# Optimization experiments

Hardware: AMD Instinct MI355X
Metric: run time of the kernel (lower is better)

The kernel has to match this reference:

```python
import jax, jax.numpy as jnp
import numpy as np

B, P, N, H, W = 8, 4096, 1024, 1024, 1024


def setup_inputs() -> dict:
    key = jax.random.key(0)
    k1, k2, k3, k4 = jax.random.split(key, 4)
    return {
        "pred_points": jax.random.uniform(k1, (B, P, 2), dtype=jnp.float32),
        "dicts_coords": jax.random.uniform(k2, (B, N, 2), dtype=jnp.float32),
        "dicts_keys": jax.random.randint(k3, (B, N), 0, 1024, dtype=jnp.int64) if jax.config.jax_enable_x64 else jax.random.randint(k3, (B, N), 0, 1024).astype(jnp.int32),
        "masks": jax.random.randint(k4, (B, H, W), 0, 1025).astype(jnp.int32),
    }


def _match_single(U, V, keys, lm):
    # U: [P,2] normalized points, V: [N,2] gt coords, keys: [N] ids, lm: [H,W] label map
    h, w = lm.shape
    x = jnp.clip(jnp.round(U[:, 0] * h).astype(jnp.int32), 0, h - 1)
    y = jnp.clip(jnp.round(U[:, 1] * w).astype(jnp.int32), 0, w - 1)
    labels = lm[x, y]                                   # [P] label at each point
    # inside[j, p] == (mask for gt j covers point p); mask j is label channel keys[j]+1
    inside = labels[None, :] == (keys + 1)[:, None]     # [N,P] bool
    # full euclidean distance matrix gt->points
    D = jnp.sqrt(jnp.sum((V[:, None, :] - U[None, :, :]) ** 2, axis=-1))  # [N,P]
    inside_any = inside.any(axis=0)                     # points inside ANY mask
    avail0 = inside_any
    bg0 = ~inside_any                                   # background points
    idx = jnp.arange(U.shape[0])
    BIG = jnp.asarray(1e30, D.dtype)

    def step(carry, xs):
        avail, bg = carry
        ins_j, d_j = xs
        cand = ins_j & avail
        cnt = cand.sum()
        d_in = jnp.where(cand, d_j, BIG)
        u_in = jnp.argmin(d_in)                         # first-index tiebreak, like list order
        d_bg = jnp.where(bg, d_j, BIG)
        u_bg = jnp.argmin(d_bg)
        has_bg = bg.any()
        use_in = cnt > 0
        u = jnp.where(use_in, u_in, jnp.where(has_bg, u_bg, -1))
        cost = jnp.where(use_in, d_in[u_in], jnp.where(has_bg, d_bg[u_bg], jnp.asarray(0.0, D.dtype)))
        # inside-match consumes u from available; multi-point case dumps others into bg
        avail = jnp.where(use_in, avail & (idx != u_in), avail)
        others = cand & (idx != u_in)
        bg = jnp.where(use_in,
                       jnp.where(cnt > 1, bg | others, bg),
                       jnp.where(has_bg, bg & (idx != u_bg), bg))
        return (avail, bg), (u, cost)

    _, (src, costs) = jax.lax.scan(step, (avail0, bg0), (inside, D))
    tgt = jnp.where(src >= 0, jnp.arange(V.shape[0]), -1)
    return src, tgt, costs.sum()


def reference(pred_points, dicts_coords, dicts_keys, masks):
    # Returns padded matches per batch: src[b,j] = matched point index for gt j (-1 if skipped),
    # tgt[b,j] = j when matched else -1, total_cost[b] = sum of matched distances.
    src, tgt, total_cost = jax.vmap(_match_single)(pred_points, dicts_coords, dicts_keys, masks)
    return src, tgt, total_cost
```

## Files before the change

kernel.cpp:

```cpp
#include <hip/hip_runtime.h>
#include <stdint.h>

#define PPTS 4096
#define NGT  1024
#define HH   1024
#define WW   1024
#define EVPOOL_CAP 3072
#define BGCAP 160
#define RB 12

#define PART_BYTES (8 * 8 * 1025 * 2)
#define LAB_OFF    PART_BYTES
#define SPILL_OFF  (LAB_OFF + 8 * PPTS * 2)
#define SPILL_CAP  2048
#define WS_NEED    (SPILL_OFF + 8 * SPILL_CAP * 2)

typedef unsigned long long u64;

__device__ __forceinline__ float pdist2(float vx, float vy, float ux, float uy) {
    float dx = __fsub_rn(vx, ux);
    float dy = __fsub_rn(vy, uy);
    return __fadd_rn(__fmul_rn(dx, dx), __fmul_rn(dy, dy));
}

__global__ __launch_bounds__(512) void label_kernel(
    const float* __restrict__ pred, const int* __restrict__ masks,
    unsigned short* __restrict__ part, unsigned short* __restrict__ labs)
{
    __shared__ int lh[1025];
    const int blk = blockIdx.x, b = blk >> 3, sb = blk & 7;
    const int t = threadIdx.x;
    lh[t] = 0; lh[t + 512] = 0;
    if (t == 0) lh[1024] = 0;
    __syncthreads();
    const int p = (sb << 9) + t;
    float2 u = ((const float2*)(pred + (size_t)b * PPTS * 2))[p];
    int xi = (int)rintf(__fmul_rn(u.x, 1024.0f));
    int yi = (int)rintf(__fmul_rn(u.y, 1024.0f));
    xi = min(max(xi, 0), HH - 1);
    yi = min(max(yi, 0), WW - 1);
    int lab = (masks + (size_t)b * HH * WW)[xi * WW + yi];
    labs[(size_t)b * PPTS + p] = (unsigned short)lab;
    atomicAdd(&lh[lab], 1);
    __syncthreads();
    unsigned short* Pp = part + (size_t)b * 8200;
    Pp[t * 8 + sb] = (unsigned short)lh[t];
    Pp[(t + 512) * 8 + sb] = (unsigned short)lh[t + 512];
    if (t == 0) Pp[1024 * 8 + sb] = (unsigned short)lh[1024];
}

__global__ __launch_bounds__(1024) void matcher_kernel(
    const float* __restrict__ pred,
    const float* __restrict__ coords,
    const int*   __restrict__ keys,
    const int*   __restrict__ masks,
    float* __restrict__ out,
    const unsigned short* __restrict__ part, const unsigned short* __restrict__ labs,
    unsigned short* __restrict__ spill, int useWs, int B)
{
    __shared__ __align__(16) char regU[32768];
    __shared__ __align__(8)  char regE[8192];
    __shared__ __align__(8)  char regB[8200];
    __shared__ __align__(8)  char regP[2 * EVPOOL_CAP];
    __shared__ __align__(4)  char regS[384];
    __shared__ __align__(8)  char regT[2048];
    __shared__ u64            wScr64[16];
    __shared__ u64            sTot;
    __shared__ unsigned short evAx[1024];
    __shared__ unsigned short occList[NGT];
    __shared__ short          matchU[NGT];
    __shared__ unsigned       bgbits[PPTS / 32];
    __shared__ int            scal[4];
    __shared__ float2         vLds[NGT];
    __shared__ unsigned       cellCnt[1024];
    __shared__ unsigned short cellOf[PPTS];
    __shared__ unsigned short gIdx[PPTS];
    __shared__ unsigned short gP[PPTS];
    __shared__ __align__(16) float2 gC[PPTS];

    float2*         bucketC  = (float2*)regU;
    unsigned short* ldsEnt   = (unsigned short*)regE;
    int*            bEnd     = (int*)regB;
    int*            occA     = ((int*)regB) + 1025;
    u64*            specWin  = (u64*)regB;
    int*            firstOcc = (int*)regP;
    unsigned short* evPool   = (unsigned short*)regP;
    unsigned*       present  = (unsigned*)regS;
    unsigned short* bgListSh = (unsigned short*)regS;
    unsigned short* bSt      = (unsigned short*)regT;
    float2*         vSteps   = (float2*)regT;
    int*   wScrI = (int*)wScr64;
    float* wScrF = (float*)wScr64;

    const int b = blockIdx.x;
    const int t = threadIdx.x;
    const int lane = t & 63, wv = t >> 6;
    const float* Ub = pred   + (size_t)b * PPTS * 2;
    const float2* Ub2 = (const float2*)Ub;
    const float* Vb = coords + (size_t)b * NGT * 2;
    const float2* Vb2 = (const float2*)Vb;
    const int*   Kb = keys   + (size_t)b * NGT;
    unsigned short* evSpillB = spill + (size_t)b * SPILL_CAP;
    const int spillCap = useWs ? SPILL_CAP : 0;

    if (t < PPTS / 32) bgbits[t] = 0;
    if (t == 0) scal[0] = 0;
    cellCnt[t] = 0;
    const int k1 = Kb[t] + 1;
    const float2 vMe = Vb2[t];
    vLds[t] = vMe;
    int lab[4]; float2 up[4];
    #pragma unroll
    for (int i = 0; i < 4; i++) up[i] = Ub2[t + (i << 10)];
    occA[t] = 0; firstOcc[t] = 0x7FFFFFFF;
    if (t == 0) { occA[1024] = 0; firstOcc[1024] = 0x7FFFFFFF; }
    if (t < 33) present[t] = 0;
    if (useWs) {
        const unsigned short* Pb = part + (size_t)b * 8200;
        const uint4 pv = reinterpret_cast<const uint4*>(Pb)[t];
        int s = (int)(pv.x & 0xFFFFu) + (int)(pv.x >> 16)
              + (int)(pv.y & 0xFFFFu) + (int)(pv.y >> 16)
              + (int)(pv.z & 0xFFFFu) + (int)(pv.z >> 16)
              + (int)(pv.w & 0xFFFFu) + (int)(pv.w >> 16);
        bEnd[t] = s;
        if (t == 0) {
            const uint4 p1 = reinterpret_cast<const uint4*>(Pb)[1024];
            bEnd[1024] = (int)(p1.x & 0xFFFFu) + (int)(p1.x >> 16)
                       + (int)(p1.y & 0xFFFFu) + (int)(p1.y >> 16)
                       + (int)(p1.z & 0xFFFFu) + (int)(p1.z >> 16)
                       + (int)(p1.w & 0xFFFFu) + (int)(p1.w >> 16);
        }
        const unsigned short* Lb = labs + (size_t)b * PPTS;
        #pragma unroll
        for (int i = 0; i < 4; i++) lab[i] = Lb[t + (i << 10)];
    } else {
        bEnd[t] = 0;
        if (t == 0) bEnd[1024] = 0;
    }
    __syncthreads();
    atomicOr(&present[k1 >> 5], 1u << (k1 & 31));
    atomicAdd(&occA[k1], 1);
    atomicMin(&firstOcc[k1], t);
    if (!useWs) {
        const int* Mb = masks + (size_t)b * HH * WW;
        #pragma unroll
        for (int i = 0; i < 4; i++) {
            float2 u = up[i];
            int xi = (int)rintf(__fmul_rn(u.x, 1024.0f));
            int yi = (int)rintf(__fmul_rn(u.y, 1024.0f));
            xi = min(max(xi, 0), HH - 1);
            yi = min(max(yi, 0), WW - 1);
            lab[i] = Mb[xi * WW + yi];
            atomicAdd(&bEnd[lab[i]], 1);
        }
    }
    __syncthreads();

    {
        int c0 = bEnd[t], o0 = occA[t];
        bool pr0 = (present[t >> 5] >> (t & 31)) & 1u;
        int bCnt = bEnd[k1];
        int fo   = firstOcc[k1];
        int evc  = (fo == t && bCnt > 0) ? (bCnt - 1) : 0;
        u64 myv = (pr0 ? ((u64)(unsigned)c0 << 32) : ((u64)(unsigned)c0 << 48))
                  | ((u64)(unsigned)evc << 16) | (u64)(unsigned)o0;
        u64 add1 = 0; bool pr1 = false;
        if (t == 1023) {
            int c1 = bEnd[1024], o1 = occA[1024];
            pr1 = present[32] & 1u;
            add1 = (pr1 ? ((u64)(unsigned)c1 << 32) : ((u64)(unsigned)c1 << 48))
                   | (u64)(unsigned)o1;
        }
        u64 tot = myv + add1;
        u64 inc = tot;
        #pragma unroll
        for (int off = 1; off < 64; off <<= 1) {
            u64 n = __shfl_up(inc, off, 64);
            if (lane >= off) inc += n;
        }
        if (lane == 63) wScr64[wv] = inc;
        __syncthreads();
        if (t < 16) {
            u64 v = wScr64[t], inc2 = v;
            #pragma unroll
            for (int off = 1; off < 16; off <<= 1) {
                u64 n = __shfl_up(inc2, off, 64);
                if (t >= off) inc2 += n;
            }
            wScr64[t] = inc2 - v;
            if (t == 15) sTot = inc2;
        }
        __syncthreads();
        u64 excl = wScr64[wv] + inc - tot;
        int nBg0v = (int)(sTot >> 48);
        int bgS = (int)(excl >> 48);
        int prS = (int)((excl >> 32) & 0xFFFF);
        int evS = (int)((excl >> 16) & 0xFFFF);
        int ocS = (int)(excl & 0xFFFF);
        int start0 = pr0 ? (nBg0v + prS) : bgS;
        bEnd[t] = start0;
        occA[t] = ocS;
        evAx[t] = (unsigned short)evS;
        if (t >= 1) bSt[t - 1] = (unsigned short)start0;
        if (t == 1023) {
            u64 ex1 = excl + myv;
            int bgS1 = (int)(ex1 >> 48);
            int prS1 = (int)((ex1 >> 32) & 0xFFFF);
            int start1 = pr1 ? (nBg0v + prS1) : bgS1;
            bEnd[1024] = start1; occA[1024] = (int)(ex1 & 0xFFFF);
            bSt[1023] = (unsigned short)start1;
        }
    }
    __syncthreads();
    const int nBg0  = (int)(sTot >> 48);
    const int totEv = (int)((sTot >> 16) & 0xFFFF);
    const int EVcap = min(EVPOOL_CAP, PPTS - nBg0);

    #pragma unroll
    for (int i = 0; i < 4; i++) {
        int p = t + (i << 10);
        int slot = atomicAdd(&bEnd[lab[i]], 1);
        ldsEnt[slot] = (unsigned short)p;
        bucketC[slot] = up[i];
        if (!((present[lab[i] >> 5] >> (lab[i] & 31)) & 1u)) {
            int cx = min(31, max(0, (int)__fmul_rn(up[i].x, 32.0f)));
            int cy = min(31, max(0, (int)__fmul_rn(up[i].y, 32.0f)));
            int cell = (cx << 5) | cy;
            cellOf[slot] = (unsigned short)cell;
            atomicAdd(&cellCnt[cell], 1u);
        }
    }
    {
        int slot = atomicAdd(&occA[k1], 1);
        occList[slot] = (unsigned short)t;
    }
    __syncthreads();

    float costPartial = 0.0f;
    {
        const int l = t + 1;
        const int os = occA[t], oe = occA[l];
        for (int i = os + 1; i < oe; i++) {
            unsigned short v = occList[i];
            int k = i - 1;
            while (k >= os && occList[k] > v) { occList[k + 1] = occList[k]; k--; }
            occList[k + 1] = v;
        }
        const int bs = bSt[t], be = bEnd[l];
        const int bn = be - bs;
        if (oe > os && bn > 0 && bn <= RB) {
            float rcx[RB], rcy[RB]; int rp[RB];
            #pragma unroll
            for (int k = 0; k < RB; k++)
                if (k < bn) { float2 c = bucketC[bs + k]; rcx[k] = c.x; rcy[k] = c.y;
                              rp[k] = ldsEnt[bs + k]; }
            unsigned cons = 0;
            for (int o = os; o < oe; o++) {
                int j = occList[o];
                float2 v = vLds[j];
                u64 best = ~0ull;
                #pragma unroll
                for (int k = 0; k < RB; k++) {
                    if (k < bn && !((cons >> k) & 1u)) {
                        float d2 = pdist2(v.x, v.y, rcx[k], rcy[k]);
                        u64 pk = ((u64)__float_as_uint(d2) << 24)
                                 | ((u64)(unsigned)rp[k] << 12) | (u64)(unsigned)k;
                        if (pk < best) best = pk;
                    }
                }
                if (best != ~0ull) {
                    int eW = (int)(best & 0xFFFull);
                    matchU[j] = (short)((best >> 12) & 0xFFFull);
                    costPartial = __fadd_rn(costPartial,
                        __fsqrt_rn(__uint_as_float((unsigned)(best >> 24))));
                    cons |= 1u << eW;
                    if (o == os) {
                        int base = evAx[j];
                        #pragma unroll
                        for (int k = 0; k < RB; k++) {
                            if (k < bn && k != eW) {
                                int idx = base + k - (k > eW ? 1 : 0);
                                if (idx < EVcap) evPool[idx] = (unsigned short)(bs + k);
                                else if (idx - EVcap < spillCap)
                                    evSpillB[idx - EVcap] = (unsigned short)rp[k];
                            }
                        }
                    }
                } else matchU[j] = -2;
            }
        } else if (oe > os) {
            u64 cons = 0;
            for (int o = os; o < oe; o++) {
                int j = occList[o];
                float2 v = vLds[j];
                u64 best = ~0ull;
                int avail = 0;
                for (int e = bs; e < be; e++) {
                    int eIdx = e - bs;
                    int p = ldsEnt[e];
                    bool consd;
                    if (eIdx < 64) consd = (cons >> eIdx) & 1ull;
                    else {
                        consd = false;
                        for (int o2 = os; o2 < o; o2++)
                            if ((int)matchU[occList[o2]] == p) { consd = true; break; }
                    }
                    if (consd) continue;
                    avail++;
                    float2 u = bucketC[e];
                    float d2 = pdist2(v.x, v.y, u.x, u.y);
                    u64 pk = ((u64)__float_as_uint(d2) << 24) | ((u64)(unsigned)p << 12)
                             | (u64)(unsigned)eIdx;
                    if (pk < best) best = pk;
                }
                if (avail > 0) {
                    int eW = (int)(best & 0xFFFull);
                    matchU[j] = (short)((best >> 12) & 0xFFFull);
                    costPartial = __fadd_rn(costPartial,
                        __fsqrt_rn(__uint_as_float((unsigned)(best >> 24))));
                    if (eW < 64) cons |= 1ull << eW;
                    if (o == os) {
                        int base = evAx[j], w3 = 0;
                        for (int e = bs; e < be; e++) {
                            if (e - bs == eW) continue;
                            int idx = base + w3;
                            if (idx < EVcap) evPool[idx] = (unsigned short)e;
                            else if (idx - EVcap < spillCap)
                                evSpillB[idx - EVcap] = ldsEnt[e];
                            w3++;
                        }
                    }
                } else matchU[j] = -2;
            }
        }
    }
    __syncthreads();

    {
        bool need = (matchU[t] == (short)-2);
        u64 m = __ballot(need);
        if (lane == 0) wScrI[wv] = __popcll(m);
    }
    __syncthreads();
    if (t < 64) {
        int orig = (t < 16) ? wScrI[t] : 0;
        int v = orig;
        #pragma unroll
        for (int off = 1; off <= 8; off <<= 1) {
            int n = __shfl_up(v, off, 64);
            if (t >= off) v += n;
        }
        if (t < 16) wScrI[t] = v - orig;
        if (t == 15) scal[0] = v;
    }
    __syncthreads();
    {
        bool need = (matchU[t] == (short)-2);
        u64 m = __ballot(need);
        if (need) {
            int rank = __popcll(m & ((1ull << lane) - 1ull));
            int idx = wScrI[wv] + rank;
            if (idx < BGCAP) { bgListSh[idx] = (unsigned short)t; vSteps[idx] = vMe; }
        }
    }
    __syncthreads();

    const int bgCnt = min(scal[0], BGCAP);
    {
        const int nStage = min(totEv, EVcap);
        float2 sc[4]; unsigned short sp[4];
        #pragma unroll
        for (int k = 0; k < 4; k++) {
            int i = t + (k << 10);
            if (i < nStage) { int slot = evPool[i]; sp[k] = ldsEnt[slot]; sc[k] = bucketC[slot]; }
        }
        __syncthreads();
        #pragma unroll
        for (int k = 0; k < 4; k++) {
            int i = t + (k << 10);
            if (i < nStage) {
                ldsEnt[nBg0 + i] = sp[k]; bucketC[nBg0 + i] = sc[k];
                int cx = min(31, max(0, (int)__fmul_rn(sc[k].x, 32.0f)));
                int cy = min(31, max(0, (int)__fmul_rn(sc[k].y, 32.0f)));
                int cell = (cx << 5) | cy;
                cellOf[nBg0 + i] = (unsigned short)cell;
                atomicAdd(&cellCnt[cell], 1u);
            }
        }
    }
    __syncthreads();

    if (bgCnt > 0) {
        const int nT = nBg0 + min(totEv, EVcap);
        {
            unsigned c0 = cellCnt[t];
            unsigned inc = c0;
            #pragma unroll
            for (int off = 1; off < 64; off <<= 1) {
                unsigned n = __shfl_up(inc, off, 64);
                if (lane >= off) inc += n;
            }
            if (lane == 63) wScrI[wv] = (int)inc;
            __syncthreads();
            if (t < 16) {
                int v = wScrI[t], inc2 = v;
                #pragma unroll
                for (int off = 1; off < 16; off <<= 1) {
                    int n = __shfl_up(inc2, off, 64);
                    if (t >= off) inc2 += n;
                }
                wScrI[t] = inc2 - v;
            }
            __syncthreads();
            unsigned excl = (unsigned)wScrI[wv] + inc - c0;
            cellCnt[t] = excl;
            __syncthreads();
        }
        #pragma unroll
        for (int k = 0; k < 4; k++) {
            int i = t + (k << 10);
            if (i < nT) {
                int cell = cellOf[i];
                int slot = (int)atomicAdd(&cellCnt[cell], 1u);
                gIdx[slot] = (unsigned short)i;
                gP[slot]   = ldsEnt[i];
                gC[slot]   = bucketC[i];
            }
        }
        __syncthreads();
        for (int s = wv; s < bgCnt; s += 16) {
            const int js = bgListSh[s];
            const float2 v = vSteps[s];
            const int lim = nBg0 + min((int)evAx[js], EVcap);
            const int cx = min(31, max(0, (int)__fmul_rn(v.x, 32.0f)));
            const int cy = min(31, max(0, (int)__fmul_rn(v.y, 32.0f)));
            u64 best = ~0ull;
            if (lane < 25) {
                int x = cx + (lane / 5) - 2, y = cy + (lane % 5) - 2;
                if ((unsigned)x < 32u && (unsigned)y < 32u) {
                    int c = (x << 5) | y;
                    int beg = c ? (int)cellCnt[c - 1] : 0;
                    int end = (int)cellCnt[c];
                    for (int i2 = beg; i2 < end; i2++) {
                        if (gIdx[i2] < lim) {
                            float2 cc = gC[i2];
                            float d2 = pdist2(v.x, v.y, cc.x, cc.y);
                            u64 pk = ((u64)__float_as_uint(d2) << 32) | gP[i2];
                            if (pk < best) best = pk;
                        }
                    }
                }
            }
            #pragma unroll
            for (int off = 32; off >= 1; off >>= 1) {
                u64 o = __shfl_xor(best, off, 64);
                if (o < best) best = o;
            }
            for (int r = 3; r <= 31; r++) {
                float gap = __fmul_rn((float)(r - 1), 0.03125f) - 1e-6f;
                float bd2 = __uint_as_float((unsigned)(best >> 32));
                if (bd2 < __fmul_rn(gap, gap)) break;
                const int ncells = 8 * r;
                for (int ci = lane; ci < ncells; ci += 64) {
                    int dx, dy;
                    if (ci < 2 * r)           { dx = -r + ci;            dy = -r; }
                    else if (ci < 4 * r)      { dx = r;                  dy = -r + (ci - 2 * r); }
                    else if (ci < 6 * r)      { dx = r - (ci - 4 * r);   dy = r; }
                    else                      { dx = -r;                 dy = r - (ci - 6 * r); }
                    int x = cx + dx, y = cy + dy;
                    if ((unsigned)x < 32u && (unsigned)y < 32u) {
                        int c = (x << 5) | y;
                        int beg = c ? (int)cellCnt[c - 1] : 0;
                        int end = (int)cellCnt[c];
                        for (int i2 = beg; i2 < end; i2++) {
                            if (gIdx[i2] < lim) {
                                float2 cc = gC[i2];
                                float d2 = pdist2(v.x, v.y, cc.x, cc.y);
                                u64 pk = ((u64)__float_as_uint(d2) << 32) | gP[i2];
                                if (pk < best) best = pk;
                            }
                        }
                    }
                }
                #pragma unroll
                for (int off = 32; off >= 1; off >>= 1) {
                    u64 o = __shfl_xor(best, off, 64);
                    if (o < best) best = o;
                }
            }
            const int ne = evAx[js];
            if (ne > EVcap && spillCap > 0) {
                for (int ei = EVcap + lane; ei < ne; ei += 64) {
                    if (ei - EVcap >= spillCap) break;
                    unsigned p = evSpillB[ei - EVcap];
                    float2 c = Ub2[p];
                    float d2 = pdist2(v.x, v.y, c.x, c.y);
                    u64 pk = ((u64)__float_as_uint(d2) << 32) | p;
                    if (pk < best) best = pk;
                }
                #pragma unroll
                for (int off = 32; off >= 1; off >>= 1) {
                    u64 o = __shfl_xor(best, off, 64);
                    if (o < best) best = o;
                }
            }
            if (lane == 0) specWin[s] = best;
        }
    }
    __syncthreads();

    {
        int done = 0;
        for (;;) {
            if (t == 0) scal[3] = bgCnt;
            __syncthreads();
            if (t >= done && t < bgCnt) {
                u64 w = specWin[t];
                if (w != ~0ull) {
                    unsigned p = (unsigned)(w & 0xFFFFFFFFull);
                    bool inval = (bgbits[p >> 5] >> (p & 31)) & 1u;
                    if (!inval) {
                        for (int s2 = done; s2 < t; s2++) {
                            u64 w2 = specWin[s2];
                            if (w2 != ~0ull &&
                                (unsigned)(w2 & 0xFFFFFFFFull) == p) { inval = true; break; }
                        }
                    }
                    if (inval) atomicMin(&scal[3], t);
                }
            }
            __syncthreads();
            const int fs = scal[3];
            if (fs >= bgCnt) break;
            if (t >= done && t < fs) {
                u64 w = specWin[t];
                if (w != ~0ull) {
                    unsigned p = (unsigned)(w & 0xFFFFFFFFull);
                    atomicOr(&bgbits[p >> 5], 1u << (p & 31));
                }
            }
            __syncthreads();
            {
                const int js = bgListSh[fs];
                const float2 v = vSteps[fs];
                const int ne = evAx[js];
                const int lim = nBg0 + min(ne, EVcap);
                u64 best = ~0ull;
                for (int i = t; i < lim; i += 1024) {
                    unsigned p = ldsEnt[i];
                    if (!((bgbits[p >> 5] >> (p & 31)) & 1u)) {
                        float2 c = bucketC[i];
                        float d2 = pdist2(v.x, v.y, c.x, c.y);
                        u64 pk = ((u64)__float_as_uint(d2) << 32) | p;
                        if (pk < best) best = pk;
                    }
                }
                for (int ei = EVcap + t; ei < ne; ei += 1024) {
                    if (ei - EVcap >= spillCap) break;
                    unsigned p = evSpillB[ei - EVcap];
                    if (!((bgbits[p >> 5] >> (p & 31)) & 1u)) {
                        float2 c = Ub2[p];
                        float d2 = pdist2(v.x, v.y, c.x, c.y);
                        u64 pk = ((u64)__float_as_uint(d2) << 32) | p;
                        if (pk < best) best = pk;
                    }
                }
                #pragma unroll
                for (int off = 32; off >= 1; off >>= 1) {
                    u64 o = __shfl_xor(best, off, 64);
                    if (o < best) best = o;
                }
                if (lane == 0) wScr64[wv] = best;
                __syncthreads();
                if (t == 0) {
                    u64 bb = wScr64[0];
                    for (int i = 1; i < 16; i++) if (wScr64[i] < bb) bb = wScr64[i];
                    specWin[fs] = bb;
                    if (bb != ~0ull) {
                        unsigned p = (unsigned)(bb & 0xFFFFFFFFull);
                        bgbits[p >> 5] |= 1u << (p & 31);
                    }
                }
            }
            done = fs + 1;
        }
    }
    if (t < bgCnt) {
        const int js = bgListSh[t];
        u64 w0 = specWin[t];
        if (w0 == ~0ull) matchU[js] = -1;
        else {
            matchU[js] = (short)(w0 & 0xFFFFFFFFull);
            costPartial = __fadd_rn(costPartial,
                __fsqrt_rn(__uint_as_float((unsigned)(w0 >> 32))));
        }
    }
    __syncthreads();

    {
        float cp = costPartial;
        #pragma unroll
        for (int off = 32; off >= 1; off >>= 1) cp += __shfl_xor(cp, off, 64);
        if (lane == 0) wScrF[wv] = cp;
    }
    __syncthreads();
    if (t == 0) {
        float tot = 0.0f;
        for (int i = 0; i < 16; ++i) tot = __fadd_rn(tot, wScrF[i]);
        out[(size_t)2 * B * NGT + b] = tot;
    }
    {
        int u = matchU[t];
        out[(size_t)b * NGT + t] = (float)u;
        out[(size_t)B * NGT + (size_t)b * NGT + t] = (u >= 0) ? (float)t : -1.0f;
    }
}

extern "C" void kernel_launch(void* const* d_in, const int* in_sizes, int n_in,
                              void* d_out, int out_size, void* d_ws, size_t ws_size,
                              hipStream_t stream) {
    const float* pred   = (const float*)d_in[0];
    const float* coords = (const float*)d_in[1];
    const int*   keys   = (const int*)d_in[2];
    const int*   masks  = (const int*)d_in[3];
    float* out = (float*)d_out;
    int B = in_sizes[2] / NGT;
    int useWs = (B == 8 && ws_size >= (size_t)WS_NEED) ? 1 : 0;
    unsigned short* partP  = (unsigned short*)d_ws;
    unsigned short* labsP  = (unsigned short*)((char*)d_ws + LAB_OFF);
    unsigned short* spillP = (unsigned short*)((char*)d_ws + SPILL_OFF);
    if (useWs) {
        label_kernel<<<B * 8, 512, 0, stream>>>(pred, masks, partP, labsP);
    }
    matcher_kernel<<<B, 1024, 0, stream>>>(pred, coords, keys, masks, out,
                                           partP, labsP, spillP, useWs, B);
}
```

Before: 110.3 us.

## Fold label gather and histogram into matcher kernel, drop separate label pass

Removes the separate label_kernel launch and its workspace round-trip. The matcher now gathers mask labels itself, issuing the gathers early so they overlap the shared-memory initialisation, and builds the label histogram with shared atomics. It also reuses the per-lane ballot rank instead of recomputing the ballot. The cost is that the random mask gathers now run on only 8 blocks instead of 64, which may expose more latency.

After: 112.7 us. 2.2% more time.

```diff
diff --git a/kernel.cpp b/kernel.cpp
--- a/kernel.cpp
+++ b/kernel.cpp
@@ -9,11 +9,8 @@
 #define BGCAP 160
 #define RB 12
 
-#define PART_BYTES (8 * 8 * 1025 * 2)
-#define LAB_OFF    PART_BYTES
-#define SPILL_OFF  (LAB_OFF + 8 * PPTS * 2)
 #define SPILL_CAP  2048
-#define WS_NEED    (SPILL_OFF + 8 * SPILL_CAP * 2)
+#define WS_NEED    (8 * SPILL_CAP * 2)
 
 typedef unsigned long long u64;
 
@@ -21,32 +18,6 @@
     float dx = __fsub_rn(vx, ux);
     float dy = __fsub_rn(vy, uy);
     return __fadd_rn(__fmul_rn(dx, dx), __fmul_rn(dy, dy));
-}
-
-__global__ __launch_bounds__(512) void label_kernel(
-    const float* __restrict__ pred, const int* __restrict__ masks,
-    unsigned short* __restrict__ part, unsigned short* __restrict__ labs)
-{
-    __shared__ int lh[1025];
-    const int blk = blockIdx.x, b = blk >> 3, sb = blk & 7;
-    const int t = threadIdx.x;
-    lh[t] = 0; lh[t + 512] = 0;
-    if (t == 0) lh[1024] = 0;
-    __syncthreads();
-    const int p = (sb << 9) + t;
-    float2 u = ((const float2*)(pred + (size_t)b * PPTS * 2))[p];
-    int xi = (int)rintf(__fmul_rn(u.x, 1024.0f));
-    int yi = (int)rintf(__fmul_rn(u.y, 1024.0f));
-    xi = min(max(xi, 0), HH - 1);
-    yi = min(max(yi, 0), WW - 1);
-    int lab = (masks + (size_t)b * HH * WW)[xi * WW + yi];
-    labs[(size_t)b * PPTS + p] = (unsigned short)lab;
-    atomicAdd(&lh[lab], 1);
-    __syncthreads();
-    unsigned short* Pp = part + (size_t)b * 8200;
-    Pp[t * 8 + sb] = (unsigned short)lh[t];
-    Pp[(t + 512) * 8 + sb] = (unsigned short)lh[t + 512];
-    if (t == 0) Pp[1024 * 8 + sb] = (unsigned short)lh[1024];
 }
 
 __global__ __launch_bounds__(1024) void matcher_kernel(
@@ -55,8 +26,7 @@
     const int*   __restrict__ keys,
     const int*   __restrict__ masks,
     float* __restrict__ out,
-    const unsigned short* __restrict__ part, const unsigned short* __restrict__ labs,
-    unsigned short* __restrict__ spill, int useWs, int B)
+    unsigned short* __restrict__ spill, int spillCap, int B)
 {
     __shared__ __align__(16) char regU[32768];
     __shared__ __align__(8)  char regE[8192];
@@ -101,59 +71,37 @@
     const float2* Vb2 = (const float2*)Vb;
     const int*   Kb = keys   + (size_t)b * NGT;
     unsigned short* evSpillB = spill + (size_t)b * SPILL_CAP;
-    const int spillCap = useWs ? SPILL_CAP : 0;
-
+
+    int lab[4]; float2 up[4];
+    #pragma unroll
+    for (int i = 0; i < 4; i++) up[i] = Ub2[t + (i << 10)];
+    const int k1v = Kb[t];
+    const float2 vMe = Vb2[t];
+    const int* Mb = masks + (size_t)b * HH * WW;
+    #pragma unroll
+    for (int i = 0; i < 4; i++) {
+        int xi = (int)rintf(__fmul_rn(up[i].x, 1024.0f));
+        int yi = (int)rintf(__fmul_rn(up[i].y, 1024.0f));
+        xi = min(max(xi, 0), HH - 1);
+        yi = min(max(yi, 0), WW - 1);
+        lab[i] = Mb[xi * WW + yi];
+    }
+    const int k1 = k1v + 1;
     if (t < PPTS / 32) bgbits[t] = 0;
     if (t == 0) scal[0] = 0;
     cellCnt[t] = 0;
-    const int k1 = Kb[t] + 1;
-    const float2 vMe = Vb2[t];
     vLds[t] = vMe;
-    int lab[4]; float2 up[4];
-    #pragma unroll
-    for (int i = 0; i < 4; i++) up[i] = Ub2[t + (i << 10)];
     occA[t] = 0; firstOcc[t] = 0x7FFFFFFF;
-    if (t == 0) { occA[1024] = 0; firstOcc[1024] = 0x7FFFFFFF; }
+    bEnd[t] = 0;
+    if (t == 0) { occA[1024] = 0; firstOcc[1024] = 0x7FFFFFFF; bEnd[1024] = 0; }
     if (t < 33) present[t] = 0;
-    if (useWs) {
-        const unsigned short* Pb = part + (size_t)b * 8200;
-        const uint4 pv = reinterpret_cast<const uint4*>(Pb)[t];
-        int s = (int)(pv.x & 0xFFFFu) + (int)(pv.x >> 16)
-              + (int)(pv.y & 0xFFFFu) + (int)(pv.y >> 16)
-              + (int)(pv.z & 0xFFFFu) + (int)(pv.z >> 16)
-              + (int)(pv.w & 0xFFFFu) + (int)(pv.w >> 16);
-        bEnd[t] = s;
-        if (t == 0) {
-            const uint4 p1 = reinterpret_cast<const uint4*>(Pb)[1024];
-            bEnd[1024] = (int)(p1.x & 0xFFFFu) + (int)(p1.x >> 16)
-                       + (int)(p1.y & 0xFFFFu) + (int)(p1.y >> 16)
-                       + (int)(p1.z & 0xFFFFu) + (int)(p1.z >> 16)
-                       + (int)(p1.w & 0xFFFFu) + (int)(p1.w >> 16);
-        }
-        const unsigned short* Lb = labs + (size_t)b * PPTS;
-        #pragma unroll
-        for (int i = 0; i < 4; i++) lab[i] = Lb[t + (i << 10)];
-    } else {
-        bEnd[t] = 0;
-        if (t == 0) bEnd[1024] = 0;
-    }
-    __syncthreads();
+    __syncthreads();
+
     atomicOr(&present[k1 >> 5], 1u << (k1 & 31));
     atomicAdd(&occA[k1], 1);
     atomicMin(&firstOcc[k1], t);
-    if (!useWs) {
-        const int* Mb = masks + (size_t)b * HH * WW;
-        #pragma unroll
-        for (int i = 0; i < 4; i++) {
-            float2 u = up[i];
-            int xi = (int)rintf(__fmul_rn(u.x, 1024.0f));
-            int yi = (int)rintf(__fmul_rn(u.y, 1024.0f));
-            xi = min(max(xi, 0), HH - 1);
-            yi = min(max(yi, 0), WW - 1);
-            lab[i] = Mb[xi * WW + yi];
-            atomicAdd(&bEnd[lab[i]], 1);
-        }
-    }
+    #pragma unroll
+    for (int i = 0; i < 4; i++) atomicAdd(&bEnd[lab[i]], 1);
     __syncthreads();
 
     {
@@ -336,9 +284,12 @@
     }
     __syncthreads();
 
-    {
-        bool need = (matchU[t] == (short)-2);
+    int myRank;
+    bool need;
+    {
+        need = (matchU[t] == (short)-2);
         u64 m = __ballot(need);
+        myRank = need ? __popcll(m & ((1ull << lane) - 1ull)) : 0;
         if (lane == 0) wScrI[wv] = __popcll(m);
     }
     __syncthreads();
@@ -354,14 +305,9 @@
         if (t == 15) scal[0] = v;
     }
     __syncthreads();
-    {
-        bool need = (matchU[t] == (short)-2);
-        u64 m = __ballot(need);
-        if (need) {
-            int rank = __popcll(m & ((1ull << lane) - 1ull));
-            int idx = wScrI[wv] + rank;
-            if (idx < BGCAP) { bgListSh[idx] = (unsigned short)t; vSteps[idx] = vMe; }
-        }
+    if (need) {
+        int idx = wScrI[wv] + myRank;
+        if (idx < BGCAP) { bgListSh[idx] = (unsigned short)t; vSteps[idx] = vMe; }
     }
     __syncthreads();
 
@@ -625,13 +571,8 @@
     const int*   masks  = (const int*)d_in[3];
     float* out = (float*)d_out;
     int B = in_sizes[2] / NGT;
-    int useWs = (B == 8 && ws_size >= (size_t)WS_NEED) ? 1 : 0;
-    unsigned short* partP  = (unsigned short*)d_ws;
-    unsigned short* labsP  = (unsigned short*)((char*)d_ws + LAB_OFF);
-    unsigned short* spillP = (unsigned short*)((char*)d_ws + SPILL_OFF);
-    if (useWs) {
-        label_kernel<<<B * 8, 512, 0, stream>>>(pred, masks, partP, labsP);
-    }
+    int spillCap = (ws_size >= (size_t)WS_NEED) ? SPILL_CAP : 0;
+    unsigned short* spillP = (unsigned short*)d_ws;
     matcher_kernel<<<B, 1024, 0, stream>>>(pred, coords, keys, masks, out,
-                                           partP, labsP, spillP, useWs, B);
+                                           spillP, spillCap, B);
 }
```
